# Performance work log

Hardware: AMD Instinct MI355X
Metric: run time of the kernel (lower is better)

## Reference

```python
import jax, jax.numpy as jnp
import numpy as np

B, N_ATOM, N_TOK = 1, 1536, 384
C_ATOM, C_PAIR, C_TOK = 128, 16, 384
C_HID, H, L = 32, 4, 3
HID = 2 * C_ATOM  # n_transition = 2
N_QUERY, N_KEY, INF = 32, 128, 1e9


def _ln(x, gamma=None, beta=None, eps=1e-5):
    mu = jnp.mean(x, axis=-1, keepdims=True)
    var = jnp.mean(jnp.square(x - mu), axis=-1, keepdims=True)
    y = (x - mu) * jax.lax.rsqrt(var + eps)
    if gamma is not None:
        y = y * gamma
    if beta is not None:
        y = y + beta
    return y


def _adaln(a, s, gamma_s, Wg, bg, Ws):
    an = _ln(a)            # LN without affine
    sn = _ln(s, gamma_s)   # scale-only LN
    return jax.nn.sigmoid(sn @ Wg + bg) * an + sn @ Ws


def _block_mask():
    # AtomTransformer.forward: 32-query x 128-key block-local mask
    offset = N_QUERY // 2 - 0.5
    n_center = N_ATOM // N_QUERY + 1
    centers = offset + jnp.arange(n_center, dtype=jnp.float32) * N_QUERY
    idx = jnp.arange(N_ATOM, dtype=jnp.float32)[:, None]
    row = (jnp.abs(idx - centers[None, :]) < N_QUERY / 2).astype(jnp.float32)
    col = (jnp.abs(idx - centers[None, :]) < N_KEY / 2).astype(jnp.float32)
    return (row @ col.T - 1.0) * INF   # [N,N]: 0 in-window, -INF outside


def _forward(ref_pos, ref_mask, ref_element, ref_charge, ref_atom_name_chars,
             ref_space_uid, token_mask, atom_to_token_index,
             W_feats, W_ref_offset, W_inv_sq, W_valid, W_l, W_m,
             W_mlp1, W_mlp2, W_mlp3, W_out_tok,
             attn_ada_gamma_s, attn_ada_Wg, attn_ada_bg, attn_ada_Ws,
             Wq, bq, Wk, Wv, lnz_g, lnz_b, Wb, Wgate, Wo, Wsg, bsg,
             tr_ada_gamma_s, tr_ada_Wg, tr_ada_bg, tr_ada_Ws,
             tr_W1, tr_W2, tr_Wog, tr_bog, tr_Wout):
    # --- RefAtomFeatureEmbedder (AF3 Alg 5 lines 1-6) ---
    feats = jnp.concatenate([
        ref_pos, ref_mask[..., None], ref_element, ref_charge[..., None],
        ref_atom_name_chars.reshape(B, N_ATOM, -1), ref_space_uid[..., None]], axis=-1)
    cl = feats @ W_feats                                     # [B,N,C_ATOM]
    d = ref_pos[:, None, :, :] - ref_pos[:, :, None, :]      # d[l,m] = pos[m]-pos[l]
    v = (ref_space_uid[:, None, :] == ref_space_uid[:, :, None]).astype(jnp.float32)[..., None]
    plm = (d @ W_ref_offset) * v
    inv_sq = 1.0 / (1.0 + jnp.sum(d * d, axis=-1, keepdims=True))
    plm = plm + (inv_sq @ W_inv_sq) * v + (v @ W_valid) * v  # [B,N,N,C_PAIR]
    ql = cl
    # --- single -> pair conditioning + pair MLP ---
    crelu = jax.nn.relu(cl)
    plm = plm + (crelu @ W_l)[:, :, None, :] + (crelu @ W_m)[:, None, :, :]
    h = jax.nn.relu(plm) @ W_mlp1
    h = jax.nn.relu(h) @ W_mlp2
    h = jax.nn.relu(h) @ W_mlp3
    plm = plm + h
    # --- AtomTransformer (Alg 7) -> DiffusionTransformer (Alg 23) ---
    beta = _block_mask()                                     # [N,N]
    atom_mask = jnp.einsum('blt,bt->bl', atom_to_token_index, token_mask)
    mask_bias = (atom_mask - 1.0)[:, None, None, :] * INF    # [B,1,1,N]
    a, s = ql, cl
    inv_sqrt = 1.0 / np.sqrt(C_HID)
    for i in range(L):
        # AttentionPairBias (Alg 24)
        an = _adaln(a, s, attn_ada_gamma_s[i], attn_ada_Wg[i], attn_ada_bg[i], attn_ada_Ws[i])
        q = (an @ Wq[i] + bq[i]).reshape(B, N_ATOM, H, C_HID)
        k = (an @ Wk[i]).reshape(B, N_ATOM, H, C_HID)
        vv = (an @ Wv[i]).reshape(B, N_ATOM, H, C_HID)
        zb = _ln(plm, lnz_g[i], lnz_b[i]) @ Wb[i]            # [B,N,N,H]
        logits = (jnp.einsum('bqhc,bkhc->bhqk', q, k) * inv_sqrt
                  + jnp.moveaxis(zb, -1, 1) + beta[None, None] + mask_bias)
        A = jax.nn.softmax(logits, axis=-1)
        o = jnp.einsum('bhqk,bkhc->bqhc', A, vv)
        g = jax.nn.sigmoid(an @ Wgate[i]).reshape(B, N_ATOM, H, C_HID)
        o = (g * o).reshape(B, N_ATOM, H * C_HID) @ Wo[i]
        attn_out = jax.nn.sigmoid(s @ Wsg[i] + bsg[i]) * o
        # ConditionedTransitionBlock (Alg 25) on pre-attention a (Alg 23)
        tn = _adaln(a, s, tr_ada_gamma_s[i], tr_ada_Wg[i], tr_ada_bg[i], tr_ada_Ws[i])
        hh = jax.nn.silu(tn @ tr_W1[i]) * (tn @ tr_W2[i])
        tr_out = jax.nn.sigmoid(s @ tr_Wog[i] + tr_bog[i]) * (hh @ tr_Wout[i])
        a = attn_out + tr_out
    # --- mean-aggregate atoms -> tokens (Alg 5 line 15) ---
    al = jax.nn.relu(a @ W_out_tok)                          # [B,N,C_TOK]
    counts = jnp.maximum(jnp.sum(atom_to_token_index, axis=1), 1.0)
    a_tok = jnp.einsum('blt,blc->btc', atom_to_token_index, al) / counts[..., None]
    return a_tok


def setup_inputs() -> dict:
    key = jax.random.key(0)
    ks = iter(jax.random.split(key, 80))

    def nrm(shape, scale=0.02):
        return jax.random.normal(next(ks), shape, dtype=jnp.float32) * scale

    inp = {}
    inp['ref_pos'] = jax.random.normal(next(ks), (B, N_ATOM, 3), dtype=jnp.float32) * 3.0
    inp['ref_mask'] = jnp.ones((B, N_ATOM), jnp.float32)
    elem = jax.random.randint(next(ks), (B, N_ATOM), 0, 128)
    inp['ref_element'] = jax.nn.one_hot(elem, 128, dtype=jnp.float32)
    inp['ref_charge'] = jax.random.normal(next(ks), (B, N_ATOM), dtype=jnp.float32)
    chars = jax.random.randint(next(ks), (B, N_ATOM, 4), 0, 64)
    inp['ref_atom_name_chars'] = jax.nn.one_hot(chars, 64, dtype=jnp.float32)
    inp['ref_space_uid'] = jnp.broadcast_to(
        (jnp.arange(N_ATOM) // 8).astype(jnp.float32), (B, N_ATOM))
    inp['token_mask'] = jnp.ones((B, N_TOK), jnp.float32)
    tok = (jnp.arange(N_ATOM) * N_TOK) // N_ATOM  # ~4 atoms per token
    inp['atom_to_token_index'] = jnp.broadcast_to(
        jax.nn.one_hot(tok, N_TOK, dtype=jnp.float32), (B, N_ATOM, N_TOK))
    # embedder params
    inp['W_feats'] = nrm((390, C_ATOM))
    inp['W_ref_offset'] = nrm((3, C_PAIR))
    inp['W_inv_sq'] = nrm((1, C_PAIR))
    inp['W_valid'] = nrm((1, C_PAIR))
    inp['W_l'] = nrm((C_ATOM, C_PAIR))
    inp['W_m'] = nrm((C_ATOM, C_PAIR))
    inp['W_mlp1'] = nrm((C_PAIR, C_PAIR))
    inp['W_mlp2'] = nrm((C_PAIR, C_PAIR))
    inp['W_mlp3'] = nrm((C_PAIR, C_PAIR))
    inp['W_out_tok'] = nrm((C_ATOM, C_TOK))
    # DiffusionTransformer params, stacked over L blocks
    inp['attn_ada_gamma_s'] = jnp.ones((L, C_ATOM), jnp.float32)
    inp['attn_ada_Wg'] = nrm((L, C_ATOM, C_ATOM))
    inp['attn_ada_bg'] = jnp.zeros((L, C_ATOM), jnp.float32)
    inp['attn_ada_Ws'] = nrm((L, C_ATOM, C_ATOM))
    inp['Wq'] = nrm((L, C_ATOM, H * C_HID))
    inp['bq'] = jnp.zeros((L, H * C_HID), jnp.float32)
    inp['Wk'] = nrm((L, C_ATOM, H * C_HID))
    inp['Wv'] = nrm((L, C_ATOM, H * C_HID))
    inp['lnz_g'] = jnp.ones((L, C_PAIR), jnp.float32)
    inp['lnz_b'] = jnp.zeros((L, C_PAIR), jnp.float32)
    inp['Wb'] = nrm((L, C_PAIR, H))
    inp['Wgate'] = nrm((L, C_ATOM, H * C_HID))
    inp['Wo'] = nrm((L, H * C_HID, C_ATOM))
    inp['Wsg'] = nrm((L, C_ATOM, C_ATOM))
    inp['bsg'] = jnp.full((L, C_ATOM), -2.0, jnp.float32)
    inp['tr_ada_gamma_s'] = jnp.ones((L, C_ATOM), jnp.float32)
    inp['tr_ada_Wg'] = nrm((L, C_ATOM, C_ATOM))
    inp['tr_ada_bg'] = jnp.zeros((L, C_ATOM), jnp.float32)
    inp['tr_ada_Ws'] = nrm((L, C_ATOM, C_ATOM))
    inp['tr_W1'] = nrm((L, C_ATOM, HID))
    inp['tr_W2'] = nrm((L, C_ATOM, HID))
    inp['tr_Wog'] = nrm((L, C_ATOM, C_ATOM))
    inp['tr_bog'] = jnp.full((L, C_ATOM), -2.0, jnp.float32)
    inp['tr_Wout'] = nrm((L, HID, C_ATOM))
    return inp


def reference(ref_pos, ref_mask, ref_element, ref_charge, ref_atom_name_chars,
              ref_space_uid, token_mask, atom_to_token_index,
              W_feats, W_ref_offset, W_inv_sq, W_valid, W_l, W_m,
              W_mlp1, W_mlp2, W_mlp3, W_out_tok,
              attn_ada_gamma_s, attn_ada_Wg, attn_ada_bg, attn_ada_Ws,
              Wq, bq, Wk, Wv, lnz_g, lnz_b, Wb, Wgate, Wo, Wsg, bsg,
              tr_ada_gamma_s, tr_ada_Wg, tr_ada_bg, tr_ada_Ws,
              tr_W1, tr_W2, tr_Wog, tr_bog, tr_Wout):
    return _forward(ref_pos, ref_mask, ref_element, ref_charge, ref_atom_name_chars,
                    ref_space_uid, token_mask, atom_to_token_index,
                    W_feats, W_ref_offset, W_inv_sq, W_valid, W_l, W_m,
                    W_mlp1, W_mlp2, W_mlp3, W_out_tok,
                    attn_ada_gamma_s, attn_ada_Wg, attn_ada_bg, attn_ada_Ws,
                    Wq, bq, Wk, Wv, lnz_g, lnz_b, Wb, Wgate, Wo, Wsg, bsg,
                    tr_ada_gamma_s, tr_ada_Wg, tr_ada_bg, tr_ada_Ws,
                    tr_W1, tr_W2, tr_Wog, tr_bog, tr_Wout)
```

## Files before the change

### kernel.cpp

```cpp
#include <hip/hip_runtime.h>
#include <math.h>

#define N_ATOM 1536
#define NLAYER 3
#define NC     196608L
#define ZSTRIDE 786432L

struct GD { const float* A; const float* B; float* C; const float* ks; const float* bias;
            const float* sg; const float* ad; int act; int ldb; int ldc; int mode; };
struct GB { GD g[18]; };

__global__ __launch_bounds__(128) void embed_tok_kernel(
    const float* __restrict__ pos, const float* __restrict__ rmask,
    const float* __restrict__ elem, const float* __restrict__ charge,
    const float* __restrict__ chars, const float* __restrict__ uid,
    const float* __restrict__ Wf, const float* __restrict__ W_l, const float* __restrict__ W_m,
    const float* __restrict__ a2t, const float* __restrict__ tmask,
    float* __restrict__ cl, float* __restrict__ aa,
    float* __restrict__ pl, float* __restrict__ pm,
    int* __restrict__ tok, float* __restrict__ amask)
{
  int l = blockIdx.x, c = threadIdx.x;
  __shared__ int sidx[6];
  __shared__ float crow[128];
  if (elem[(long)l * 128 + c] > 0.5f) sidx[0] = c;
  float v0 = chars[(long)l * 256 + c];
  if (v0 > 0.5f) sidx[1 + (c >> 6)] = c & 63;
  float v1 = chars[(long)l * 256 + 128 + c];
  if (v1 > 0.5f) sidx[3 + (c >> 6)] = c & 63;
  for (int j = c; j < 384; j += 128)
    if (a2t[(long)l * 384 + j] > 0.5f) sidx[5] = j;
  __syncthreads();
  float acc = pos[l * 3 + 0] * Wf[c]
            + pos[l * 3 + 1] * Wf[128 + c]
            + pos[l * 3 + 2] * Wf[256 + c]
            + rmask[l] * Wf[384 + c]
            + Wf[(4 + sidx[0]) * 128 + c]
            + charge[l] * Wf[132 * 128 + c]
            + Wf[(133 + sidx[1]) * 128 + c]
            + Wf[(197 + sidx[2]) * 128 + c]
            + Wf[(261 + sidx[3]) * 128 + c]
            + Wf[(325 + sidx[4]) * 128 + c]
            + uid[l] * Wf[389 * 128 + c];
  long gi = (long)l * 128 + c;
  cl[gi] = acc; aa[gi] = acc; crow[c] = fmaxf(acc, 0.f);
  __syncthreads();
  if (c < 32) {
    const float* W = (c < 16) ? W_l : W_m;
    int o = c & 15;
    float s = 0.f;
    for (int cc = 0; cc < 128; cc++) s = fmaf(crow[cc], W[cc * 16 + o], s);
    if (c < 16) pl[l * 16 + o] = s; else pm[l * 16 + o] = s;
  }
  if (c == 127) {
    int j = sidx[5];
    tok[l] = j; amask[l] = tmask[j];
  }
}

__device__ __forceinline__ void gemm64_body(float* sm, const GD d, int row0, int col0) {
  float* As = sm; float* Bs = sm + 2176;
  float* rmu = sm + 4352;
  float* rsd = sm + 4416;
  int tid = threadIdx.x;
  if (d.mode >= 1) {
    int r = tid >> 2, sgi = tid & 3;
    const float* Ar = d.A + (long)(row0 + r) * 128 + sgi * 32;
    float4 vv[8];
    float s1 = 0.f;
#pragma unroll
    for (int c4 = 0; c4 < 8; c4++) {
      vv[c4] = *(const float4*)(Ar + c4 * 4);
      s1 += vv[c4].x + vv[c4].y + vv[c4].z + vv[c4].w;
    }
    s1 += __shfl_xor(s1, 1); s1 += __shfl_xor(s1, 2);
    float mu = s1 * (1.f / 128.f);
    float s2 = 0.f;
#pragma unroll
    for (int c4 = 0; c4 < 8; c4++) {
      float dx = vv[c4].x - mu, dy = vv[c4].y - mu, dz = vv[c4].z - mu, dw = vv[c4].w - mu;
      s2 += dx * dx + dy * dy + dz * dz + dw * dw;
    }
    s2 += __shfl_xor(s2, 1); s2 += __shfl_xor(s2, 2);
    if (sgi == 0) {
      rmu[r] = mu;
      rsd[r] = rsqrtf(s2 * (1.f / 128.f) + 1e-5f);
    }
  }
  int tx = tid & 15, ty = tid >> 4;
  float acc[4][4] = {};
  for (int k0 = 0; k0 < 128; k0 += 32) {
    __syncthreads();
    { int r = tid >> 3, k4 = tid & 7;
#pragma unroll
      for (int half = 0; half < 2; half++) {
        int row = r + half * 32;
        long gro = (long)(row0 + row) * 128 + k0 + k4 * 4;
        float4 v = *(const float4*)(d.A + gro);
        float vals[4] = {v.x, v.y, v.z, v.w};
        if (d.mode >= 1) {
          float mu = rmu[row], sd = rsd[row];
          if (d.mode == 2) {
            float4 sg4 = *(const float4*)(d.sg + gro);
            float4 ad4 = *(const float4*)(d.ad + gro);
            vals[0] = fmaf(sg4.x, (vals[0] - mu) * sd, ad4.x);
            vals[1] = fmaf(sg4.y, (vals[1] - mu) * sd, ad4.y);
            vals[2] = fmaf(sg4.z, (vals[2] - mu) * sd, ad4.z);
            vals[3] = fmaf(sg4.w, (vals[3] - mu) * sd, ad4.w);
          } else {
#pragma unroll
            for (int cc = 0; cc < 4; cc++) vals[cc] = (vals[cc] - mu) * sd;
          }
        }
        if (d.ks) {
          const float* kp = d.ks + k0 + k4 * 4;
#pragma unroll
          for (int cc = 0; cc < 4; cc++) vals[cc] *= kp[cc];
        }
        As[(k4 * 4 + 0) * 68 + row] = vals[0]; As[(k4 * 4 + 1) * 68 + row] = vals[1];
        As[(k4 * 4 + 2) * 68 + row] = vals[2]; As[(k4 * 4 + 3) * 68 + row] = vals[3];
      } }
    { int kk = tid >> 4, n4 = tid & 15;
#pragma unroll
      for (int half = 0; half < 2; half++) {
        int k = kk + half * 16;
        *(float4*)&Bs[k * 68 + n4 * 4] = *(const float4*)(d.B + (long)(k0 + k) * d.ldb + col0 + n4 * 4);
      } }
    __syncthreads();
#pragma unroll
    for (int kk = 0; kk < 32; kk++) {
      float4 a = *(const float4*)&As[kk * 68 + ty * 4];
      float4 b = *(const float4*)&Bs[kk * 68 + tx * 4];
      float av[4] = {a.x, a.y, a.z, a.w}, bv[4] = {b.x, b.y, b.z, b.w};
#pragma unroll
      for (int i = 0; i < 4; i++)
#pragma unroll
        for (int j = 0; j < 4; j++) acc[i][j] = fmaf(av[i], bv[j], acc[i][j]);
    }
  }
  __syncthreads();
#pragma unroll
  for (int i = 0; i < 4; i++) {
    int row = row0 + ty * 4 + i;
#pragma unroll
    for (int j = 0; j < 4; j++) {
      int col = col0 + tx * 4 + j;
      float x = acc[i][j];
      if (d.bias) x += d.bias[col];
      if (d.act == 1) x = 1.f / (1.f + expf(-x));
      else if (d.act == 2) x = fmaxf(x, 0.f);
      d.C[(long)row * d.ldc + col] = x;
    }
  }
}

__global__ __launch_bounds__(256) void gemm64(GB args)
{
  __shared__ __align__(16) float sm[4480];
  gemm64_body(sm, args.g[blockIdx.z], blockIdx.y * 64, blockIdx.x * 64);
}

__global__ __launch_bounds__(256) void zpre_kernel(
    const float* __restrict__ pos, const float* __restrict__ uid,
    const float* __restrict__ Wro, const float* __restrict__ Winv, const float* __restrict__ Wval,
    const float* __restrict__ M1, const float* __restrict__ M2, const float* __restrict__ M3,
    const float* __restrict__ Lg, const float* __restrict__ Lb, const float* __restrict__ Wb,
    const float* __restrict__ pl, const float* __restrict__ pm, float* __restrict__ zb,
    GB ba)
{
  __shared__ __align__(16) float sm[4480];
  int bid = blockIdx.x, tid = threadIdx.x;
  if (bid < 864) {
    GD d = ba.g[bid / 48];
    int tt = bid % 48;
    gemm64_body(sm, d, (tt >> 1) * 64, (tt & 1) * 64);
    return;
  }
  int zbid = bid - 864;
  if (tid < 48)  sm[tid] = Wro[tid];
  if (tid < 16)  { sm[48 + tid] = Winv[tid]; sm[64 + tid] = Wval[tid]; }
  sm[80 + tid] = M1[tid]; sm[336 + tid] = M2[tid]; sm[592 + tid] = M3[tid];
  if (tid < 48)  { sm[848 + tid] = Lg[tid]; sm[896 + tid] = Lb[tid]; }
  if (tid < 192) sm[944 + tid] = Wb[tid];
  __syncthreads();
  const float* sWro = sm;      const float* sWinv = sm + 48;  const float* sWval = sm + 64;
  const float* sM1 = sm + 80;  const float* sM2 = sm + 336;   const float* sM3 = sm + 592;
  const float* sLg = sm + 848; const float* sLb = sm + 896;   const float* sWb = sm + 944;
  int b = zbid >> 4;
  int pc = (zbid & 15) * 256 + tid;
  int qi = pc >> 7, kj = pc & 127;
  int l = b * 32 + qi, m = b * 32 - 48 + kj;
  long base = (long)(b * 32 + qi) * 128 + kj;
  if (m < 0 || m >= N_ATOM) {
    for (int i = 0; i < NLAYER; i++)
      for (int h = 0; h < 4; h++) zb[i * ZSTRIDE + h * NC + base] = 0.f;
    return;
  }
  float dx = pos[m * 3 + 0] - pos[l * 3 + 0];
  float dy = pos[m * 3 + 1] - pos[l * 3 + 1];
  float dz = pos[m * 3 + 2] - pos[l * 3 + 2];
  float v = (uid[m] == uid[l]) ? 1.f : 0.f;
  float inv = 1.f / (1.f + dx * dx + dy * dy + dz * dz);
  float pv[16], ha[16], hb[16];
#pragma unroll
  for (int j = 0; j < 16; j++)
    pv[j] = v * (dx * sWro[j] + dy * sWro[16 + j] + dz * sWro[32 + j] + inv * sWinv[j] + sWval[j])
            + pl[l * 16 + j] + pm[m * 16 + j];
#pragma unroll
  for (int jo = 0; jo < 16; jo++) { float s = 0.f; for (int ji = 0; ji < 16; ji++) s = fmaf(fmaxf(pv[ji], 0.f), sM1[ji * 16 + jo], s); ha[jo] = s; }
#pragma unroll
  for (int jo = 0; jo < 16; jo++) { float s = 0.f; for (int ji = 0; ji < 16; ji++) s = fmaf(fmaxf(ha[ji], 0.f), sM2[ji * 16 + jo], s); hb[jo] = s; }
#pragma unroll
  for (int jo = 0; jo < 16; jo++) { float s = 0.f; for (int ji = 0; ji < 16; ji++) s = fmaf(fmaxf(hb[ji], 0.f), sM3[ji * 16 + jo], s); ha[jo] = s; }
#pragma unroll
  for (int j = 0; j < 16; j++) pv[j] += ha[j];
  for (int i = 0; i < NLAYER; i++) {
    float mu = 0.f;
#pragma unroll
    for (int j = 0; j < 16; j++) mu += pv[j];
    mu *= (1.f / 16.f);
    float var = 0.f;
#pragma unroll
    for (int j = 0; j < 16; j++) { float dd = pv[j] - mu; var += dd * dd; }
    var *= (1.f / 16.f);
    float rs = rsqrtf(var + 1e-5f);
    float zn[16];
#pragma unroll
    for (int j = 0; j < 16; j++) zn[j] = (pv[j] - mu) * rs * sLg[i * 16 + j] + sLb[i * 16 + j];
    for (int h = 0; h < 4; h++) {
      float s = 0.f;
#pragma unroll
      for (int j = 0; j < 16; j++) s = fmaf(zn[j], sWb[i * 64 + j * 4 + h], s);
      zb[i * ZSTRIDE + h * NC + base] = s;
    }
  }
}

__global__ __launch_bounds__(256) void attn_tr_kernel(
    const float* __restrict__ qb, const float* __restrict__ kb, const float* __restrict__ vb,
    const float* __restrict__ gb, const float* __restrict__ zb, const float* __restrict__ amask,
    float* __restrict__ go,
    const float* __restrict__ h1, const float* __restrict__ h2, const float* __restrict__ B2,
    const float* __restrict__ g2, float* __restrict__ trbuf)
{
  __shared__ __align__(16) float sm[11904];
  int bid = blockIdx.x, t = threadIdx.x;
  if (bid < 96) {
    int u = bid;
    int row0 = (u >> 1) * 32, col0 = (u & 1) * 64;
    float* As = sm; float* Bs = sm + 1152;
    int tx = t & 15, ty = t >> 4;
    float acc2[2][4] = {};
    for (int k0 = 0; k0 < 256; k0 += 32) {
      __syncthreads();
      { int r = t >> 3, k4 = t & 7;
        long o = (long)(row0 + r) * 256 + k0 + k4 * 4;
        float4 x = *(const float4*)(h1 + o);
        float4 y = *(const float4*)(h2 + o);
        As[(k4 * 4 + 0) * 36 + r] = (x.x / (1.f + expf(-x.x))) * y.x;
        As[(k4 * 4 + 1) * 36 + r] = (x.y / (1.f + expf(-x.y))) * y.y;
        As[(k4 * 4 + 2) * 36 + r] = (x.z / (1.f + expf(-x.z))) * y.z;
        As[(k4 * 4 + 3) * 36 + r] = (x.w / (1.f + expf(-x.w))) * y.w;
      }
      for (int e = t; e < 512; e += 256) {
        int k = e >> 4, n4 = e & 15;
        *(float4*)&Bs[k * 68 + n4 * 4] = *(const float4*)(B2 + (long)(k0 + k) * 128 + col0 + n4 * 4);
      }
      __syncthreads();
#pragma unroll
      for (int kk = 0; kk < 32; kk++) {
        float a0 = As[kk * 36 + ty * 2], a1 = As[kk * 36 + ty * 2 + 1];
        float4 b = *(const float4*)&Bs[kk * 68 + tx * 4];
        float bv[4] = {b.x, b.y, b.z, b.w};
#pragma unroll
        for (int j = 0; j < 4; j++) {
          acc2[0][j] = fmaf(a0, bv[j], acc2[0][j]);
          acc2[1][j] = fmaf(a1, bv[j], acc2[1][j]);
        }
      }
    }
#pragma unroll
    for (int i = 0; i < 2; i++) {
      long o = (long)(row0 + ty * 2 + i) * 128 + col0 + tx * 4;
      float4 g4 = *(const float4*)(g2 + o);
      float4 r;
      r.x = g4.x * acc2[i][0]; r.y = g4.y * acc2[i][1];
      r.z = g4.z * acc2[i][2]; r.w = g4.w * acc2[i][3];
      *(float4*)(trbuf + o) = r;
    }
    return;
  }
  float* qs = sm;
  float* ks = sm + 576;
  float* vs = sm + 5184;
  float* ps = sm + 9792;
  int u = bid - 96;
  int h = u / 96, bx = u - h * 96;
  int b = bx >> 1, half = bx & 1;
  int q0 = b * 32 + half * 16;
  int kbase = b * 32 - 48;
  const float* zbh = zb + (long)h * NC;
  if (t < 128) {
    int qi = t >> 3, c4 = t & 7;
    *(float4*)&qs[qi * 36 + c4 * 4] = *(const float4*)(qb + (long)(q0 + qi) * 128 + h * 32 + c4 * 4);
  }
  for (int idx = t; idx < 128 * 8; idx += 256) {
    int kj = idx >> 3, c4 = idx & 7;
    int m = kbase + kj;
    float4 kv = make_float4(0.f, 0.f, 0.f, 0.f), vv = make_float4(0.f, 0.f, 0.f, 0.f);
    if (m >= 0 && m < N_ATOM) {
      kv = *(const float4*)(kb + (long)m * 128 + h * 32 + c4 * 4);
      vv = *(const float4*)(vb + (long)m * 128 + h * 32 + c4 * 4);
    }
    *(float4*)&ks[kj * 36 + c4 * 4] = kv;
    *(float4*)&vs[kj * 36 + c4 * 4] = vv;
  }
  __syncthreads();
  const float isq = 0.17677669529663687f;
  for (int p = t; p < 2048; p += 256) {
    int qi = p >> 7, kj = p & 127;
    int m = kbase + kj;
    float s = 0.f;
#pragma unroll
    for (int c4 = 0; c4 < 8; c4++) {
      float4 a = *(const float4*)&qs[qi * 36 + c4 * 4];
      float4 k4 = *(const float4*)&ks[kj * 36 + c4 * 4];
      s = fmaf(a.x, k4.x, s); s = fmaf(a.y, k4.y, s);
      s = fmaf(a.z, k4.z, s); s = fmaf(a.w, k4.w, s);
    }
    float logit;
    if (m >= 0 && m < N_ATOM) {
      logit = s * isq + zbh[(long)(q0 + qi) * 128 + kj] + (amask[m] - 1.f) * 1e9f;
    } else {
      logit = -1e9f;
    }
    ps[qi * 132 + kj] = logit;
  }
  __syncthreads();
  {
    int row = t >> 4, ln = t & 15;
    float mx = -1e30f;
    for (int kj = ln; kj < 128; kj += 16) mx = fmaxf(mx, ps[row * 132 + kj]);
#pragma unroll
    for (int o = 8; o > 0; o >>= 1) mx = fmaxf(mx, __shfl_xor(mx, o));
    float smv = 0.f;
    for (int kj = ln; kj < 128; kj += 16) { float e = expf(ps[row * 132 + kj] - mx); ps[row * 132 + kj] = e; smv += e; }
#pragma unroll
    for (int o = 8; o > 0; o >>= 1) smv += __shfl_xor(smv, o);
    float r = 1.f / smv;
    for (int kj = ln; kj < 128; kj += 16) ps[row * 132 + kj] *= r;
  }
  __syncthreads();
  {
    int qi = t >> 4, seg = (t >> 3) & 1, c4 = t & 7;
    float4 acc = make_float4(0.f, 0.f, 0.f, 0.f);
    int kj0 = seg * 64;
#pragma unroll 4
    for (int kj = kj0; kj < kj0 + 64; kj++) {
      float p = ps[qi * 132 + kj];
      float4 v = *(const float4*)&vs[kj * 36 + c4 * 4];
      acc.x = fmaf(p, v.x, acc.x); acc.y = fmaf(p, v.y, acc.y);
      acc.z = fmaf(p, v.z, acc.z); acc.w = fmaf(p, v.w, acc.w);
    }
    acc.x += __shfl_xor(acc.x, 8);
    acc.y += __shfl_xor(acc.y, 8);
    acc.z += __shfl_xor(acc.z, 8);
    acc.w += __shfl_xor(acc.w, 8);
    if (seg == 0) {
      long gi = (long)(q0 + qi) * 128 + h * 32 + c4 * 4;
      float4 g = *(const float4*)(gb + gi);
      acc.x *= g.x; acc.y *= g.y; acc.z *= g.z; acc.w *= g.w;
      *(float4*)(go + gi) = acc;
    }
  }
}

__global__ __launch_bounds__(256) void wo_kernel(
    const float* __restrict__ A1, const float* __restrict__ B1,
    const float* __restrict__ g1, const float* __restrict__ tr,
    float* __restrict__ C)
{
  __shared__ __align__(16) float As[32 * 36];
  __shared__ __align__(16) float Bs[32 * 68];
  const int N = 128;
  int t = threadIdx.x;
  int row0 = blockIdx.y * 32, col0 = blockIdx.x * 64;
  int tx = t & 15, ty = t >> 4;
  float acc1[2][4] = {};
  for (int k0 = 0; k0 < 128; k0 += 32) {
    __syncthreads();
    { int r = t >> 3, k4 = t & 7;
      float4 v = *(const float4*)(A1 + (long)(row0 + r) * 128 + k0 + k4 * 4);
      As[(k4 * 4 + 0) * 36 + r] = v.x; As[(k4 * 4 + 1) * 36 + r] = v.y;
      As[(k4 * 4 + 2) * 36 + r] = v.z; As[(k4 * 4 + 3) * 36 + r] = v.w;
    }
    for (int e = t; e < 512; e += 256) {
      int k = e >> 4, n4 = e & 15;
      *(float4*)&Bs[k * 68 + n4 * 4] = *(const float4*)(B1 + (long)(k0 + k) * N + col0 + n4 * 4);
    }
    __syncthreads();
#pragma unroll
    for (int kk = 0; kk < 32; kk++) {
      float a0 = As[kk * 36 + ty * 2], a1 = As[kk * 36 + ty * 2 + 1];
      float4 b = *(const float4*)&Bs[kk * 68 + tx * 4];
      float bv[4] = {b.x, b.y, b.z, b.w};
#pragma unroll
      for (int j = 0; j < 4; j++) {
        acc1[0][j] = fmaf(a0, bv[j], acc1[0][j]);
        acc1[1][j] = fmaf(a1, bv[j], acc1[1][j]);
      }
    }
  }
#pragma unroll
  for (int i = 0; i < 2; i++) {
    long o = (long)(row0 + ty * 2 + i) * N + col0 + tx * 4;
    float4 ga = *(const float4*)(g1 + o);
    float4 tv = *(const float4*)(tr + o);
    float4 r;
    r.x = ga.x * acc1[i][0] + tv.x;
    r.y = ga.y * acc1[i][1] + tv.y;
    r.z = ga.z * acc1[i][2] + tv.z;
    r.w = ga.w * acc1[i][3] + tv.w;
    *(float4*)(C + o) = r;
  }
}

__global__ __launch_bounds__(256) void gemm_scatter(
    const float* __restrict__ A, const float* __restrict__ B,
    const int* __restrict__ tok,
    float* __restrict__ out, int K)
{
  __shared__ __align__(16) float As[32][68];
  __shared__ __align__(16) float Bs[32][68];
  int tid = threadIdx.x;
  int row0 = blockIdx.y * 64, col0 = blockIdx.x * 64;
  int tx = tid & 15, ty = tid >> 4;
  float acc[4][4] = {};
  for (int k0 = 0; k0 < K; k0 += 32) {
    __syncthreads();
    { int r = tid >> 3, k4 = tid & 7;
#pragma unroll
      for (int half = 0; half < 2; half++) {
        int row = r + half * 32;
        float4 v = *(const float4*)(A + (long)(row0 + row) * K + k0 + k4 * 4);
        As[k4 * 4 + 0][row] = v.x; As[k4 * 4 + 1][row] = v.y;
        As[k4 * 4 + 2][row] = v.z; As[k4 * 4 + 3][row] = v.w;
      } }
    { int kk = tid >> 4, n4 = tid & 15;
#pragma unroll
      for (int half = 0; half < 2; half++) {
        int k = kk + half * 16;
        float4 v = *(const float4*)(B + (long)(k0 + k) * 384 + col0 + n4 * 4);
        *(float4*)&Bs[k][n4 * 4] = v;
      } }
    __syncthreads();
#pragma unroll
    for (int kk = 0; kk < 32; kk++) {
      float4 a = *(const float4*)&As[kk][ty * 4];
      float4 b = *(const float4*)&Bs[kk][tx * 4];
      float av[4] = {a.x, a.y, a.z, a.w}, bv[4] = {b.x, b.y, b.z, b.w};
#pragma unroll
      for (int i = 0; i < 4; i++)
#pragma unroll
        for (int j = 0; j < 4; j++) acc[i][j] = fmaf(av[i], bv[j], acc[i][j]);
    }
  }
  __syncthreads();
  int r0 = row0 + ty * 4;
  int t0 = tok[r0];
  int cnt = 0;
#pragma unroll
  for (int i = 0; i < 4; i++) cnt += (tok[r0 + i] == t0) ? 1 : 0;
  float inv = 1.f / fmaxf((float)cnt, 1.f);
#pragma unroll
  for (int j = 0; j < 4; j++) {
    int col = col0 + tx * 4 + j;
    float s = 0.f;
#pragma unroll
    for (int i = 0; i < 4; i++)
      if (tok[r0 + i] == t0) s += fmaxf(acc[i][j], 0.f);
    out[(long)t0 * 384 + col] = s * inv;
  }
}

extern "C" void kernel_launch(void* const* d_in, const int* in_sizes, int n_in,
                              void* d_out, int out_size, void* d_ws, size_t ws_size,
                              hipStream_t stream)
{
  const float* pos    = (const float*)d_in[0];
  const float* rmask  = (const float*)d_in[1];
  const float* elem   = (const float*)d_in[2];
  const float* charge = (const float*)d_in[3];
  const float* chars  = (const float*)d_in[4];
  const float* uid    = (const float*)d_in[5];
  const float* tmask  = (const float*)d_in[6];
  const float* a2t    = (const float*)d_in[7];
  const float* Wf     = (const float*)d_in[8];
  const float* Wro    = (const float*)d_in[9];
  const float* Winv   = (const float*)d_in[10];
  const float* Wval   = (const float*)d_in[11];
  const float* W_l    = (const float*)d_in[12];
  const float* W_m    = (const float*)d_in[13];
  const float* M1     = (const float*)d_in[14];
  const float* M2     = (const float*)d_in[15];
  const float* M3     = (const float*)d_in[16];
  const float* Wtok   = (const float*)d_in[17];
  const float* gA     = (const float*)d_in[18];
  const float* WgA    = (const float*)d_in[19];
  const float* bgA    = (const float*)d_in[20];
  const float* WsA    = (const float*)d_in[21];
  const float* Wq     = (const float*)d_in[22];
  const float* bq     = (const float*)d_in[23];
  const float* Wk     = (const float*)d_in[24];
  const float* Wv     = (const float*)d_in[25];
  const float* Lg     = (const float*)d_in[26];
  const float* Lb     = (const float*)d_in[27];
  const float* Wb     = (const float*)d_in[28];
  const float* Wgate  = (const float*)d_in[29];
  const float* Wo     = (const float*)d_in[30];
  const float* Wsg    = (const float*)d_in[31];
  const float* bsg    = (const float*)d_in[32];
  const float* gT     = (const float*)d_in[33];
  const float* WgT    = (const float*)d_in[34];
  const float* bgT    = (const float*)d_in[35];
  const float* WsT    = (const float*)d_in[36];
  const float* trW1   = (const float*)d_in[37];
  const float* trW2   = (const float*)d_in[38];
  const float* Wog    = (const float*)d_in[39];
  const float* bog    = (const float*)d_in[40];
  const float* Wout   = (const float*)d_in[41];
  float* out = (float*)d_out;

  float* ws = (float*)d_ws;
  size_t off = 0;
  auto alloc = [&](size_t n) { float* p = ws + off; off += n; return p; };
  float* cl     = alloc(NC);
  float* aa     = alloc(NC);
  float* qbuf   = alloc(NC);
  float* kbuf   = alloc(NC);
  float* vbuf   = alloc(NC);
  float* gbuf   = alloc(NC);
  float* gobuf  = alloc(NC);
  float* trbuf  = alloc(NC);
  float* h1     = alloc((size_t)N_ATOM * 256);
  float* h2     = alloc((size_t)N_ATOM * 256);
  float* pl     = alloc((size_t)N_ATOM * 16);
  float* pm     = alloc((size_t)N_ATOM * 16);
  float* zbias  = alloc((size_t)NLAYER * ZSTRIDE);
  float* sgA    = alloc(NC * NLAYER);
  float* adA    = alloc(NC * NLAYER);
  float* sgT    = alloc(NC * NLAYER);
  float* adT    = alloc(NC * NLAYER);
  float* gsg    = alloc(NC * NLAYER);
  float* gog    = alloc(NC * NLAYER);
  float* amask  = alloc(N_ATOM);
  int*   tok    = (int*)alloc(N_ATOM);
  (void)ws_size; (void)in_sizes; (void)n_in; (void)out_size;

  embed_tok_kernel<<<N_ATOM, 128, 0, stream>>>(pos, rmask, elem, charge, chars, uid, Wf,
                                               W_l, W_m, a2t, tmask,
                                               cl, aa, pl, pm, tok, amask);

  {
    GB ba = {};
    for (int i = 0; i < NLAYER; i++) {
      size_t o = (size_t)i * NC;
      ba.g[i * 6 + 0] = { cl, WgA + i * 16384, sgA + o, gA + i * 128, bgA + i * 128, nullptr, nullptr, 1, 128, 128, 1 };
      ba.g[i * 6 + 1] = { cl, WsA + i * 16384, adA + o, gA + i * 128, nullptr,       nullptr, nullptr, 0, 128, 128, 1 };
      ba.g[i * 6 + 2] = { cl, WgT + i * 16384, sgT + o, gT + i * 128, bgT + i * 128, nullptr, nullptr, 1, 128, 128, 1 };
      ba.g[i * 6 + 3] = { cl, WsT + i * 16384, adT + o, gT + i * 128, nullptr,       nullptr, nullptr, 0, 128, 128, 1 };
      ba.g[i * 6 + 4] = { cl, Wsg + i * 16384, gsg + o, nullptr,      bsg + i * 128, nullptr, nullptr, 1, 128, 128, 0 };
      ba.g[i * 6 + 5] = { cl, Wog + i * 16384, gog + o, nullptr,      bog + i * 128, nullptr, nullptr, 1, 128, 128, 0 };
    }
    zpre_kernel<<<768 + 864, 256, 0, stream>>>(pos, uid, Wro, Winv, Wval, M1, M2, M3,
                                               Lg, Lb, Wb, pl, pm, zbias, ba);
  }

  for (int i = 0; i < NLAYER; i++) {
    size_t o = (size_t)i * NC;
    {
      GB ba = {};
      ba.g[0] = { aa, Wq + i * 16384,        qbuf,     nullptr, bq + i * 128, sgA + o, adA + o, 0, 128, 128, 2 };
      ba.g[1] = { aa, Wk + i * 16384,        kbuf,     nullptr, nullptr,      sgA + o, adA + o, 0, 128, 128, 2 };
      ba.g[2] = { aa, Wv + i * 16384,        vbuf,     nullptr, nullptr,      sgA + o, adA + o, 0, 128, 128, 2 };
      ba.g[3] = { aa, Wgate + i * 16384,     gbuf,     nullptr, nullptr,      sgA + o, adA + o, 1, 128, 128, 2 };
      ba.g[4] = { aa, trW1 + i * 32768,       h1,      nullptr, nullptr,      sgT + o, adT + o, 0, 256, 256, 2 };
      ba.g[5] = { aa, trW1 + i * 32768 + 128, h1 + 128, nullptr, nullptr,     sgT + o, adT + o, 0, 256, 256, 2 };
      ba.g[6] = { aa, trW2 + i * 32768,       h2,      nullptr, nullptr,      sgT + o, adT + o, 0, 256, 256, 2 };
      ba.g[7] = { aa, trW2 + i * 32768 + 128, h2 + 128, nullptr, nullptr,     sgT + o, adT + o, 0, 256, 256, 2 };
      gemm64<<<dim3(2, 24, 8), 256, 0, stream>>>(ba);
    }
    attn_tr_kernel<<<480, 256, 0, stream>>>(qbuf, kbuf, vbuf, gbuf,
                                            zbias + (size_t)i * ZSTRIDE, amask, gobuf,
                                            h1, h2, Wout + i * 32768, gog + o, trbuf);
    wo_kernel<<<dim3(2, 48), 256, 0, stream>>>(gobuf, Wo + i * 16384, gsg + o, trbuf, aa);
  }

  gemm_scatter<<<dim3(6, 24), 256, 0, stream>>>(aa, Wtok, tok, out, 128);
}
```

Before: 317.4 us.

## Fuse per-layer attention, Wo and next-layer GEMMs into one kernel with atomic counters

Merges the attention/transition kernel, the Wo projection, and the next layer's projection GEMMs (or the final token scatter) into a single launch per layer. Blocks in later stages spin-wait on global atomic counters set by earlier-stage blocks instead of relying on kernel boundaries. This is meant to cut launch overhead and tail idle time between small kernels. It relies on waiting blocks not starving producer blocks of residency, so it risks deadlock or wasted spinning if scheduling order differs.

```diff
diff --git a/kernel.cpp b/kernel.cpp
--- a/kernel.cpp
+++ b/kernel.cpp
@@ -9,6 +9,33 @@
 struct GD { const float* A; const float* B; float* C; const float* ks; const float* bias;
             const float* sg; const float* ad; int act; int ldb; int ldc; int mode; };
 struct GB { GD g[18]; };
+
+struct MP {
+  float *qbuf, *kbuf, *vbuf, *gbuf, *gobuf, *trbuf, *h1, *h2, *aa;
+  const float *zbias, *amask;
+  const float *sgA, *adA, *sgT, *adT, *gsg, *gog;
+  const float *Wq, *bq, *Wk, *Wv, *Wgate, *trW1, *trW2, *Wo, *Wout, *Wtok;
+  const int *tok;
+  float *out;
+  int *ctrs;
+  int layer;
+  int has_next;
+};
+
+__device__ __forceinline__ void sig_done(int* c) {
+  __syncthreads();
+  __threadfence();
+  if (threadIdx.x == 0)
+    __hip_atomic_fetch_add(c, 1, __ATOMIC_RELEASE, __HIP_MEMORY_SCOPE_AGENT);
+}
+__device__ __forceinline__ void wait_for(int* c, int tgt) {
+  if (threadIdx.x == 0) {
+    while (__hip_atomic_load(c, __ATOMIC_ACQUIRE, __HIP_MEMORY_SCOPE_AGENT) < tgt)
+      __builtin_amdgcn_s_sleep(2);
+  }
+  __syncthreads();
+  __threadfence();
+}
 
 __global__ __launch_bounds__(128) void embed_tok_kernel(
     const float* __restrict__ pos, const float* __restrict__ rmask,
@@ -18,9 +45,10 @@
     const float* __restrict__ a2t, const float* __restrict__ tmask,
     float* __restrict__ cl, float* __restrict__ aa,
     float* __restrict__ pl, float* __restrict__ pm,
-    int* __restrict__ tok, float* __restrict__ amask)
+    int* __restrict__ tok, float* __restrict__ amask, int* __restrict__ ctrs)
 {
   int l = blockIdx.x, c = threadIdx.x;
+  if (l == 0 && c < 8) ctrs[c] = 0;
   __shared__ int sidx[6];
   __shared__ float crow[128];
   if (elem[(long)l * 128 + c] > 0.5f) sidx[0] = c;
@@ -236,81 +264,94 @@
   }
 }
 
-__global__ __launch_bounds__(256) void attn_tr_kernel(
-    const float* __restrict__ qb, const float* __restrict__ kb, const float* __restrict__ vb,
-    const float* __restrict__ gb, const float* __restrict__ zb, const float* __restrict__ amask,
-    float* __restrict__ go,
-    const float* __restrict__ h1, const float* __restrict__ h2, const float* __restrict__ B2,
-    const float* __restrict__ g2, float* __restrict__ trbuf)
-{
-  __shared__ __align__(16) float sm[11904];
-  int bid = blockIdx.x, t = threadIdx.x;
-  if (bid < 96) {
-    int u = bid;
-    int row0 = (u >> 1) * 32, col0 = (u & 1) * 64;
-    float* As = sm; float* Bs = sm + 1152;
-    int tx = t & 15, ty = t >> 4;
-    float acc2[2][4] = {};
-    for (int k0 = 0; k0 < 256; k0 += 32) {
-      __syncthreads();
-      { int r = t >> 3, k4 = t & 7;
-        long o = (long)(row0 + r) * 256 + k0 + k4 * 4;
-        float4 x = *(const float4*)(h1 + o);
-        float4 y = *(const float4*)(h2 + o);
-        As[(k4 * 4 + 0) * 36 + r] = (x.x / (1.f + expf(-x.x))) * y.x;
-        As[(k4 * 4 + 1) * 36 + r] = (x.y / (1.f + expf(-x.y))) * y.y;
-        As[(k4 * 4 + 2) * 36 + r] = (x.z / (1.f + expf(-x.z))) * y.z;
-        As[(k4 * 4 + 3) * 36 + r] = (x.w / (1.f + expf(-x.w))) * y.w;
+__device__ __forceinline__ GD make_gd(const MP& P, int i, int slot) {
+  GD d;
+  d.A = P.aa; d.ks = nullptr; d.bias = nullptr; d.act = 0; d.mode = 2;
+  long o = (long)i * NC;
+  if (slot < 4) { d.sg = P.sgA + o; d.ad = P.adA + o; d.ldb = 128; d.ldc = 128; }
+  else          { d.sg = P.sgT + o; d.ad = P.adT + o; d.ldb = 256; d.ldc = 256; }
+  switch (slot) {
+    case 0: d.B = P.Wq + i * 16384;          d.C = P.qbuf;     d.bias = P.bq + i * 128; break;
+    case 1: d.B = P.Wk + i * 16384;          d.C = P.kbuf;     break;
+    case 2: d.B = P.Wv + i * 16384;          d.C = P.vbuf;     break;
+    case 3: d.B = P.Wgate + i * 16384;       d.C = P.gbuf;     d.act = 1; break;
+    case 4: d.B = P.trW1 + i * 32768;        d.C = P.h1;       break;
+    case 5: d.B = P.trW1 + i * 32768 + 128;  d.C = P.h1 + 128; break;
+    case 6: d.B = P.trW2 + i * 32768;        d.C = P.h2;       break;
+    default:d.B = P.trW2 + i * 32768 + 128;  d.C = P.h2 + 128; break;
+  }
+  return d;
+}
+
+__device__ __forceinline__ void tr_body(float* sm, const MP& P, int layer, int u) {
+  int t = threadIdx.x;
+  int row0 = (u >> 1) * 32, col0 = (u & 1) * 64;
+  const float* B2 = P.Wout + layer * 32768;
+  const float* g2 = P.gog + (long)layer * NC;
+  float* As = sm; float* Bs = sm + 1152;
+  int tx = t & 15, ty = t >> 4;
+  float acc2[2][4] = {};
+  for (int k0 = 0; k0 < 256; k0 += 32) {
+    __syncthreads();
+    { int r = t >> 3, k4 = t & 7;
+      long o = (long)(row0 + r) * 256 + k0 + k4 * 4;
+      float4 x = *(const float4*)(P.h1 + o);
+      float4 y = *(const float4*)(P.h2 + o);
+      As[(k4 * 4 + 0) * 36 + r] = (x.x / (1.f + expf(-x.x))) * y.x;
+      As[(k4 * 4 + 1) * 36 + r] = (x.y / (1.f + expf(-x.y))) * y.y;
+      As[(k4 * 4 + 2) * 36 + r] = (x.z / (1.f + expf(-x.z))) * y.z;
+      As[(k4 * 4 + 3) * 36 + r] = (x.w / (1.f + expf(-x.w))) * y.w;
+    }
+    for (int e = t; e < 512; e += 256) {
+      int k = e >> 4, n4 = e & 15;
+      *(float4*)&Bs[k * 68 + n4 * 4] = *(const float4*)(B2 + (long)(k0 + k) * 128 + col0 + n4 * 4);
+    }
+    __syncthreads();
+#pragma unroll
+    for (int kk = 0; kk < 32; kk++) {
+      float a0 = As[kk * 36 + ty * 2], a1 = As[kk * 36 + ty * 2 + 1];
+      float4 b = *(const float4*)&Bs[kk * 68 + tx * 4];
+      float bv[4] = {b.x, b.y, b.z, b.w};
+#pragma unroll
+      for (int j = 0; j < 4; j++) {
+        acc2[0][j] = fmaf(a0, bv[j], acc2[0][j]);
+        acc2[1][j] = fmaf(a1, bv[j], acc2[1][j]);
       }
-      for (int e = t; e < 512; e += 256) {
-        int k = e >> 4, n4 = e & 15;
-        *(float4*)&Bs[k * 68 + n4 * 4] = *(const float4*)(B2 + (long)(k0 + k) * 128 + col0 + n4 * 4);
-      }
-      __syncthreads();
-#pragma unroll
-      for (int kk = 0; kk < 32; kk++) {
-        float a0 = As[kk * 36 + ty * 2], a1 = As[kk * 36 + ty * 2 + 1];
-        float4 b = *(const float4*)&Bs[kk * 68 + tx * 4];
-        float bv[4] = {b.x, b.y, b.z, b.w};
-#pragma unroll
-        for (int j = 0; j < 4; j++) {
-          acc2[0][j] = fmaf(a0, bv[j], acc2[0][j]);
-          acc2[1][j] = fmaf(a1, bv[j], acc2[1][j]);
-        }
-      }
-    }
-#pragma unroll
-    for (int i = 0; i < 2; i++) {
-      long o = (long)(row0 + ty * 2 + i) * 128 + col0 + tx * 4;
-      float4 g4 = *(const float4*)(g2 + o);
-      float4 r;
-      r.x = g4.x * acc2[i][0]; r.y = g4.y * acc2[i][1];
-      r.z = g4.z * acc2[i][2]; r.w = g4.w * acc2[i][3];
-      *(float4*)(trbuf + o) = r;
-    }
-    return;
-  }
+    }
+  }
+#pragma unroll
+  for (int i = 0; i < 2; i++) {
+    long o = (long)(row0 + ty * 2 + i) * 128 + col0 + tx * 4;
+    float4 g4 = *(const float4*)(g2 + o);
+    float4 r;
+    r.x = g4.x * acc2[i][0]; r.y = g4.y * acc2[i][1];
+    r.z = g4.z * acc2[i][2]; r.w = g4.w * acc2[i][3];
+    *(float4*)(P.trbuf + o) = r;
+  }
+}
+
+__device__ __forceinline__ void attn_body(float* sm, const MP& P, int layer, int u) {
   float* qs = sm;
   float* ks = sm + 576;
   float* vs = sm + 5184;
   float* ps = sm + 9792;
-  int u = bid - 96;
+  int t = threadIdx.x;
   int h = u / 96, bx = u - h * 96;
   int b = bx >> 1, half = bx & 1;
   int q0 = b * 32 + half * 16;
   int kbase = b * 32 - 48;
-  const float* zbh = zb + (long)h * NC;
+  const float* zbh = P.zbias + (long)layer * ZSTRIDE + (long)h * NC;
   if (t < 128) {
     int qi = t >> 3, c4 = t & 7;
-    *(float4*)&qs[qi * 36 + c4 * 4] = *(const float4*)(qb + (long)(q0 + qi) * 128 + h * 32 + c4 * 4);
+    *(float4*)&qs[qi * 36 + c4 * 4] = *(const float4*)(P.qbuf + (long)(q0 + qi) * 128 + h * 32 + c4 * 4);
   }
   for (int idx = t; idx < 128 * 8; idx += 256) {
     int kj = idx >> 3, c4 = idx & 7;
     int m = kbase + kj;
     float4 kv = make_float4(0.f, 0.f, 0.f, 0.f), vv = make_float4(0.f, 0.f, 0.f, 0.f);
     if (m >= 0 && m < N_ATOM) {
-      kv = *(const float4*)(kb + (long)m * 128 + h * 32 + c4 * 4);
-      vv = *(const float4*)(vb + (long)m * 128 + h * 32 + c4 * 4);
+      kv = *(const float4*)(P.kbuf + (long)m * 128 + h * 32 + c4 * 4);
+      vv = *(const float4*)(P.vbuf + (long)m * 128 + h * 32 + c4 * 4);
     }
     *(float4*)&ks[kj * 36 + c4 * 4] = kv;
     *(float4*)&vs[kj * 36 + c4 * 4] = vv;
@@ -330,7 +371,7 @@
     }
     float logit;
     if (m >= 0 && m < N_ATOM) {
-      logit = s * isq + zbh[(long)(q0 + qi) * 128 + kj] + (amask[m] - 1.f) * 1e9f;
+      logit = s * isq + zbh[(long)(q0 + qi) * 128 + kj] + (P.amask[m] - 1.f) * 1e9f;
     } else {
       logit = -1e9f;
     }
@@ -368,35 +409,31 @@
     acc.w += __shfl_xor(acc.w, 8);
     if (seg == 0) {
       long gi = (long)(q0 + qi) * 128 + h * 32 + c4 * 4;
-      float4 g = *(const float4*)(gb + gi);
+      float4 g = *(const float4*)(P.gbuf + gi);
       acc.x *= g.x; acc.y *= g.y; acc.z *= g.z; acc.w *= g.w;
-      *(float4*)(go + gi) = acc;
-    }
-  }
-}
-
-__global__ __launch_bounds__(256) void wo_kernel(
-    const float* __restrict__ A1, const float* __restrict__ B1,
-    const float* __restrict__ g1, const float* __restrict__ tr,
-    float* __restrict__ C)
-{
-  __shared__ __align__(16) float As[32 * 36];
-  __shared__ __align__(16) float Bs[32 * 68];
-  const int N = 128;
+      *(float4*)(P.gobuf + gi) = acc;
+    }
+  }
+}
+
+__device__ __forceinline__ void wo_body(float* sm, const MP& P, int layer, int u) {
   int t = threadIdx.x;
-  int row0 = blockIdx.y * 32, col0 = blockIdx.x * 64;
+  int row0 = (u >> 1) * 32, col0 = (u & 1) * 64;
+  const float* B1 = P.Wo + layer * 16384;
+  const float* g1 = P.gsg + (long)layer * NC;
+  float* As = sm; float* Bs = sm + 1152;
   int tx = t & 15, ty = t >> 4;
   float acc1[2][4] = {};
   for (int k0 = 0; k0 < 128; k0 += 32) {
     __syncthreads();
     { int r = t >> 3, k4 = t & 7;
-      float4 v = *(const float4*)(A1 + (long)(row0 + r) * 128 + k0 + k4 * 4);
+      float4 v = *(const float4*)(P.gobuf + (long)(row0 + r) * 128 + k0 + k4 * 4);
       As[(k4 * 4 + 0) * 36 + r] = v.x; As[(k4 * 4 + 1) * 36 + r] = v.y;
       As[(k4 * 4 + 2) * 36 + r] = v.z; As[(k4 * 4 + 3) * 36 + r] = v.w;
     }
     for (int e = t; e < 512; e += 256) {
       int k = e >> 4, n4 = e & 15;
-      *(float4*)&Bs[k * 68 + n4 * 4] = *(const float4*)(B1 + (long)(k0 + k) * N + col0 + n4 * 4);
+      *(float4*)&Bs[k * 68 + n4 * 4] = *(const float4*)(B1 + (long)(k0 + k) * 128 + col0 + n4 * 4);
     }
     __syncthreads();
 #pragma unroll
@@ -413,51 +450,45 @@
   }
 #pragma unroll
   for (int i = 0; i < 2; i++) {
-    long o = (long)(row0 + ty * 2 + i) * N + col0 + tx * 4;
+    long o = (long)(row0 + ty * 2 + i) * 128 + col0 + tx * 4;
     float4 ga = *(const float4*)(g1 + o);
-    float4 tv = *(const float4*)(tr + o);
+    float4 tv = *(const float4*)(P.trbuf + o);
     float4 r;
     r.x = ga.x * acc1[i][0] + tv.x;
     r.y = ga.y * acc1[i][1] + tv.y;
     r.z = ga.z * acc1[i][2] + tv.z;
     r.w = ga.w * acc1[i][3] + tv.w;
-    *(float4*)(C + o) = r;
-  }
-}
-
-__global__ __launch_bounds__(256) void gemm_scatter(
-    const float* __restrict__ A, const float* __restrict__ B,
-    const int* __restrict__ tok,
-    float* __restrict__ out, int K)
-{
-  __shared__ __align__(16) float As[32][68];
-  __shared__ __align__(16) float Bs[32][68];
+    *(float4*)(P.aa + o) = r;
+  }
+}
+
+__device__ __forceinline__ void scatter_body(float* sm, const MP& P, int u) {
+  float* As = sm; float* Bs = sm + 2176;
   int tid = threadIdx.x;
-  int row0 = blockIdx.y * 64, col0 = blockIdx.x * 64;
+  int row0 = (u / 6) * 64, col0 = (u % 6) * 64;
   int tx = tid & 15, ty = tid >> 4;
   float acc[4][4] = {};
-  for (int k0 = 0; k0 < K; k0 += 32) {
+  for (int k0 = 0; k0 < 128; k0 += 32) {
     __syncthreads();
     { int r = tid >> 3, k4 = tid & 7;
 #pragma unroll
       for (int half = 0; half < 2; half++) {
         int row = r + half * 32;
-        float4 v = *(const float4*)(A + (long)(row0 + row) * K + k0 + k4 * 4);
-        As[k4 * 4 + 0][row] = v.x; As[k4 * 4 + 1][row] = v.y;
-        As[k4 * 4 + 2][row] = v.z; As[k4 * 4 + 3][row] = v.w;
+        float4 v = *(const float4*)(P.aa + (long)(row0 + row) * 128 + k0 + k4 * 4);
+        As[(k4 * 4 + 0) * 68 + row] = v.x; As[(k4 * 4 + 1) * 68 + row] = v.y;
+        As[(k4 * 4 + 2) * 68 + row] = v.z; As[(k4 * 4 + 3) * 68 + row] = v.w;
       } }
     { int kk = tid >> 4, n4 = tid & 15;
 #pragma unroll
       for (int half = 0; half < 2; half++) {
         int k = kk + half * 16;
-        float4 v = *(const float4*)(B + (long)(k0 + k) * 384 + col0 + n4 * 4);
-        *(float4*)&Bs[k][n4 * 4] = v;
+        *(float4*)&Bs[k * 68 + n4 * 4] = *(const float4*)(P.Wtok + (long)(k0 + k) * 384 + col0 + n4 * 4);
       } }
     __syncthreads();
 #pragma unroll
     for (int kk = 0; kk < 32; kk++) {
-      float4 a = *(const float4*)&As[kk][ty * 4];
-      float4 b = *(const float4*)&Bs[kk][tx * 4];
+      float4 a = *(const float4*)&As[kk * 68 + ty * 4];
+      float4 b = *(const float4*)&Bs[kk * 68 + tx * 4];
       float av[4] = {a.x, a.y, a.z, a.w}, bv[4] = {b.x, b.y, b.z, b.w};
 #pragma unroll
       for (int i = 0; i < 4; i++)
@@ -467,10 +498,10 @@
   }
   __syncthreads();
   int r0 = row0 + ty * 4;
-  int t0 = tok[r0];
+  int t0 = P.tok[r0];
   int cnt = 0;
 #pragma unroll
-  for (int i = 0; i < 4; i++) cnt += (tok[r0 + i] == t0) ? 1 : 0;
+  for (int i = 0; i < 4; i++) cnt += (P.tok[r0 + i] == t0) ? 1 : 0;
   float inv = 1.f / fmaxf((float)cnt, 1.f);
 #pragma unroll
   for (int j = 0; j < 4; j++) {
@@ -478,8 +509,37 @@
     float s = 0.f;
 #pragma unroll
     for (int i = 0; i < 4; i++)
-      if (tok[r0 + i] == t0) s += fmaxf(acc[i][j], 0.f);
-    out[(long)t0 * 384 + col] = s * inv;
+      if (P.tok[r0 + i] == t0) s += fmaxf(acc[i][j], 0.f);
+    P.out[(long)t0 * 384 + col] = s * inv;
+  }
+}
+
+__global__ __launch_bounds__(256) void mega_kernel(MP P)
+{
+  __shared__ __align__(16) float sm[11904];
+  int bid = blockIdx.x;
+  int i = P.layer;
+  int* cA = P.ctrs + 2 * i;
+  int* cB = cA + 1;
+  if (bid < 96) {
+    tr_body(sm, P, i, bid);
+    sig_done(cA);
+  } else if (bid < 480) {
+    attn_body(sm, P, i, bid - 96);
+    sig_done(cA);
+  } else if (bid < 576) {
+    wait_for(cA, 480);
+    wo_body(sm, P, i, bid - 480);
+    sig_done(cB);
+  } else if (P.has_next) {
+    wait_for(cB, 96);
+    int u = bid - 576;
+    GD d = make_gd(P, i + 1, u / 48);
+    int t48 = u % 48;
+    gemm64_body(sm, d, (t48 >> 1) * 64, (t48 & 1) * 64);
+  } else {
+    wait_for(cB, 96);
+    scatter_body(sm, P, bid - 576);
   }
 }
 
@@ -555,11 +615,12 @@
   float* gog    = alloc(NC * NLAYER);
   float* amask  = alloc(N_ATOM);
   int*   tok    = (int*)alloc(N_ATOM);
+  int*   ctrs   = (int*)alloc(8);
   (void)ws_size; (void)in_sizes; (void)n_in; (void)out_size;
 
   embed_tok_kernel<<<N_ATOM, 128, 0, stream>>>(pos, rmask, elem, charge, chars, uid, Wf,
                                                W_l, W_m, a2t, tmask,
-                                               cl, aa, pl, pm, tok, amask);
+                                               cl, aa, pl, pm, tok, amask, ctrs);
 
   {
     GB ba = {};
@@ -576,25 +637,32 @@
                                                Lg, Lb, Wb, pl, pm, zbias, ba);
   }
 
+  {
+    GB ba = {};
+    ba.g[0] = { aa, Wq,          qbuf,     nullptr, bq, sgA, adA, 0, 128, 128, 2 };
+    ba.g[1] = { aa, Wk,          kbuf,     nullptr, nullptr, sgA, adA, 0, 128, 128, 2 };
+    ba.g[2] = { aa, Wv,          vbuf,     nullptr, nullptr, sgA, adA, 0, 128, 128, 2 };
+    ba.g[3] = { aa, Wgate,       gbuf,     nullptr, nullptr, sgA, adA, 1, 128, 128, 2 };
+    ba.g[4] = { aa, trW1,        h1,       nullptr, nullptr, sgT, adT, 0, 256, 256, 2 };
+    ba.g[5] = { aa, trW1 + 128,  h1 + 128, nullptr, nullptr, sgT, adT, 0, 256, 256, 2 };
+    ba.g[6] = { aa, trW2,        h2,       nullptr, nullptr, sgT, adT, 0, 256, 256, 2 };
+    ba.g[7] = { aa, trW2 + 128,  h2 + 128, nullptr, nullptr, sgT, adT, 0, 256, 256, 2 };
+    gemm64<<<dim3(2, 24, 8), 256, 0, stream>>>(ba);
+  }
+
+  MP P;
+  P.qbuf = qbuf; P.kbuf = kbuf; P.vbuf = vbuf; P.gbuf = gbuf;
+  P.gobuf = gobuf; P.trbuf = trbuf; P.h1 = h1; P.h2 = h2; P.aa = aa;
+  P.zbias = zbias; P.amask = amask;
+  P.sgA = sgA; P.adA = adA; P.sgT = sgT; P.adT = adT; P.gsg = gsg; P.gog = gog;
+  P.Wq = Wq; P.bq = bq; P.Wk = Wk; P.Wv = Wv; P.Wgate = Wgate;
+  P.trW1 = trW1; P.trW2 = trW2; P.Wo = Wo; P.Wout = Wout; P.Wtok = Wtok;
+  P.tok = tok; P.out = out; P.ctrs = ctrs;
+
   for (int i = 0; i < NLAYER; i++) {
-    size_t o = (size_t)i * NC;
-    {
-      GB ba = {};
-      ba.g[0] = { aa, Wq + i * 16384,        qbuf,     nullptr, bq + i * 128, sgA + o, adA + o, 0, 128, 128, 2 };
-      ba.g[1] = { aa, Wk + i * 16384,        kbuf,     nullptr, nullptr,      sgA + o, adA + o, 0, 128, 128, 2 };
-      ba.g[2] = { aa, Wv + i * 16384,        vbuf,     nullptr, nullptr,      sgA + o, adA + o, 0, 128, 128, 2 };
-      ba.g[3] = { aa, Wgate + i * 16384,     gbuf,     nullptr, nullptr,      sgA + o, adA + o, 1, 128, 128, 2 };
-      ba.g[4] = { aa, trW1 + i * 32768,       h1,      nullptr, nullptr,      sgT + o, adT + o, 0, 256, 256, 2 };
-      ba.g[5] = { aa, trW1 + i * 32768 + 128, h1 + 128, nullptr, nullptr,     sgT + o, adT + o, 0, 256, 256, 2 };
-      ba.g[6] = { aa, trW2 + i * 32768,       h2,      nullptr, nullptr,      sgT + o, adT + o, 0, 256, 256, 2 };
-      ba.g[7] = { aa, trW2 + i * 32768 + 128, h2 + 128, nullptr, nullptr,     sgT + o, adT + o, 0, 256, 256, 2 };
-      gemm64<<<dim3(2, 24, 8), 256, 0, stream>>>(ba);
-    }
-    attn_tr_kernel<<<480, 256, 0, stream>>>(qbuf, kbuf, vbuf, gbuf,
-                                            zbias + (size_t)i * ZSTRIDE, amask, gobuf,
-                                            h1, h2, Wout + i * 32768, gog + o, trbuf);
-    wo_kernel<<<dim3(2, 48), 256, 0, stream>>>(gobuf, Wo + i * 16384, gsg + o, trbuf, aa);
-  }
-
-  gemm_scatter<<<dim3(6, 24), 256, 0, stream>>>(aa, Wtok, tok, out, 128);
-}
+    P.layer = i;
+    P.has_next = (i < NLAYER - 1) ? 1 : 0;
+    int nblocks = P.has_next ? 960 : 720;
+    mega_kernel<<<nblocks, 256, 0, stream>>>(P);
+  }
+}
```

Measured after the change: 865.5 us. 2.73x slower.
